# Optimization experiments

Hardware: AMD Instinct MI355X
Metric: run time of the kernel (lower is better)

Reference implementation:

```python
import jax, jax.numpy as jnp
import numpy as np

B_GRAPHS = 32   # number of graphs in the batch (static)
HEADS = 8
EPS = 1e-8


def _layer_norm(x, g, b):
    mu = x.mean(-1, keepdims=True)
    var = x.var(-1, keepdims=True)
    return (x - mu) * jax.lax.rsqrt(var + 1e-5) * g + b


def setup_inputs() -> dict:
    key = jax.random.key(0)
    ks = jax.random.split(key, 16)
    N, C, d, M = 5120, 128, 16, 256
    E = N * 16
    f32 = jnp.float32
    sc_c = 1.0 / np.sqrt(C)
    inp = {
        'x': jax.random.normal(ks[0], (N, C), f32),
        'pe_re': jax.random.normal(ks[1], (N, d), f32),
        'pe_im': jax.random.normal(ks[2], (N, d), f32),
        'wq': jax.random.normal(ks[3], (C, C), f32) * sc_c,
        'bq': jnp.zeros((C,), f32),
        'wk': jax.random.normal(ks[4], (C, C), f32) * sc_c,
        'bk': jnp.zeros((C,), f32),
        'wv': jax.random.normal(ks[5], (C, C), f32) * sc_c,
        'bv': jnp.zeros((C,), f32),
        'wo': jax.random.normal(ks[6], (C, C), f32) * sc_c,
        'bo': jnp.zeros((C,), f32),
        'pe_w1': jax.random.normal(ks[7], (4 * d, 2 * d), f32) * (1.0 / np.sqrt(4 * d)),
        'pe_b1': jnp.zeros((2 * d,), f32),
        'pe_w2': jax.random.normal(ks[8], (2 * d, HEADS), f32) * (1.0 / np.sqrt(2 * d)),
        'pe_b2': jnp.zeros((HEADS,), f32),
        'mlp_w1': jax.random.normal(ks[9], (C, 2 * C), f32) * sc_c,
        'mlp_b1': jnp.zeros((2 * C,), f32),
        'mlp_w2': jax.random.normal(ks[10], (2 * C, C), f32) * (1.0 / np.sqrt(2 * C)),
        'mlp_b2': jnp.zeros((C,), f32),
        'ln2_g': jnp.ones((C,), f32),
        'ln2_b': jnp.zeros((C,), f32),
        'ln3_g': jnp.ones((C,), f32),
        'ln3_b': jnp.zeros((C,), f32),
        'batch': jnp.sort(jax.random.randint(ks[11], (N,), 0, B_GRAPHS, jnp.int32)),
        'edge_index': jax.random.randint(ks[12], (2, E), 0, N, jnp.int32),
        'nmax': M,
    }
    return inp


def reference(x, pe_re, pe_im, wq, bq, wk, bk, wv, bv, wo, bo,
              pe_w1, pe_b1, pe_w2, pe_b2, mlp_w1, mlp_b1, mlp_w2, mlp_b2,
              ln2_g, ln2_b, ln3_g, ln3_b, batch, edge_index, nmax):
    N, C = x.shape
    H = HEADS
    dh = C // H
    M = nmax

    # --- to_dense_batch: ragged [N,*] -> dense [B, M, *] + mask ---
    counts = jax.ops.segment_sum(jnp.ones((N,), jnp.int32), batch, num_segments=B_GRAPHS)
    offsets = jnp.concatenate([jnp.zeros((1,), jnp.int32), jnp.cumsum(counts)[:-1]])
    intra = jnp.arange(N, dtype=jnp.int32) - offsets[batch]
    hd = jnp.zeros((B_GRAPHS, M, C), x.dtype).at[batch, intra].set(x)
    ar = jnp.zeros((B_GRAPHS, M, pe_re.shape[1]), x.dtype).at[batch, intra].set(pe_re)
    ai = jnp.zeros((B_GRAPHS, M, pe_im.shape[1]), x.dtype).at[batch, intra].set(pe_im)
    mask = jnp.zeros((B_GRAPHS, M), bool).at[batch, intra].set(True)

    # --- pairwise complex-angle PE bias ---
    pn = jnp.sqrt(ar * ar + ai * ai + EPS)                 # [B,M,d] complex_norm
    denom = pn[:, :, None, :] * pn[:, None, :, :] + EPS    # [B,M,M,d]
    # z_i * conj(z_j) normalized -> cos/sin of pairwise angle
    real = (ar[:, :, None, :] * ar[:, None, :, :] + ai[:, :, None, :] * ai[:, None, :, :]) / denom
    imag = (ai[:, :, None, :] * ar[:, None, :, :] - ar[:, :, None, :] * ai[:, None, :, :]) / denom
    pni = jnp.broadcast_to(pn[:, :, None, :], real.shape)
    pnj = jnp.broadcast_to(pn[:, None, :, :], real.shape)
    bias_in = jnp.concatenate([pni, pnj, real, imag], axis=-1)       # [B,M,M,4d]
    hb = jax.nn.relu(bias_in @ pe_w1 + pe_b1) @ pe_w2 + pe_b2        # [B,M,M,H]
    # torch: bias.transpose(1,-1) swaps dims 1 and 3 -> [B,H,M,M]
    bias = jnp.transpose(hb, (0, 3, 2, 1))                           # [B,H,q,k]

    # --- multi-head attention with float bias + key padding mask ---
    q = (hd @ wq + bq).reshape(B_GRAPHS, M, H, dh)
    k = (hd @ wk + bk).reshape(B_GRAPHS, M, H, dh)
    v = (hd @ wv + bv).reshape(B_GRAPHS, M, H, dh)
    scores = jnp.einsum('bihd,bjhd->bhij', q, k) / np.sqrt(dh) + bias
    scores = jnp.where(mask[:, None, None, :], scores, -1e9)
    attn = jax.nn.softmax(scores, axis=-1)
    o = jnp.einsum('bhij,bjhd->bihd', attn, v).reshape(B_GRAPHS, M, C)
    o = o @ wo + bo

    # --- back to ragged, residual, norms, FFN ---
    h = o[batch, intra] + x
    h = _layer_norm(h, ln2_g, ln2_b)
    out = h + (jax.nn.relu(h @ mlp_w1 + mlp_b1) @ mlp_w2 + mlp_b2)
    out = _layer_norm(out, ln3_g, ln3_b)
    return out
```

## Files before the change

kernel.cpp:

```cpp
#include <hip/hip_runtime.h>

#define N_NODES 5120
#define C_DIM   128
#define D_PE    16
#define M_MAX   256
#define B_G     32
#define H_HEADS 8
#define DH      16
#define EPS_PE  1e-8f
#define QT      4
#define SCP     264

#define WS_COUNTS   0
#define WS_OFFSETS  32
#define WS_INTRA    64
#define WS_MASK     5184
#define WS_HD       13376
#define WS_AR       1061952
#define WS_AI       1193024
#define WS_PN       1324096
#define WS_CN       1455168
#define WS_KFHI     1717312
#define WS_KFLO     1979456
#define WS_Q        2110528
#define WS_K        3159104
#define WS_V        4207680
#define WS_OATT     5256256
#define WS_OPROJ    6304832
#define WS_HLN      7353408
#define WS_FFNH     8008768
#define WS_FFNO     9319488
#define WS_BIAS     9974848
#define WS_ZERO_FLOATS 1324096

typedef __attribute__((ext_vector_type(8))) short bf8_t;
typedef __attribute__((ext_vector_type(4))) float f4_t;

__device__ inline short f2bf(float f) {
    union { float f; unsigned u; } v; v.f = f;
    unsigned r = (v.u + 0x7FFF + ((v.u >> 16) & 1)) >> 16;
    return (short)r;
}
__device__ inline float bf2f(short h) {
    union { unsigned u; float f; } v; v.u = ((unsigned)(unsigned short)h) << 16;
    return v.f;
}
__device__ inline unsigned pack2(short a, short b) {
    return (unsigned)(unsigned short)a | ((unsigned)(unsigned short)b << 16);
}
__device__ inline bf8_t bf8_from2(uint2 a, uint2 b) {
    bf8_t o;
    o[0]=(short)a.x; o[1]=(short)(a.x>>16); o[2]=(short)a.y; o[3]=(short)(a.y>>16);
    o[4]=(short)b.x; o[5]=(short)(b.x>>16); o[6]=(short)b.y; o[7]=(short)(b.y>>16);
    return o;
}

__global__ __launch_bounds__(256) void setup_kernel(
    const int* __restrict__ batch, int* __restrict__ offsets, int* __restrict__ intra)
{
    __shared__ int cnt[B_G];
    __shared__ int off[B_G];
    const int t = threadIdx.x;
    if (t < B_G) cnt[t] = 0;
    __syncthreads();
    for (int n = t; n < N_NODES; n += 256) atomicAdd(&cnt[batch[n]], 1);
    __syncthreads();
    if (t == 0) { int s = 0; for (int b = 0; b < B_G; ++b) { off[b] = s; s += cnt[b]; } }
    __syncthreads();
    if (t < B_G) offsets[t] = off[t];
    for (int n = t; n < N_NODES; n += 256) intra[n] = n - off[batch[n]];
}

__global__ __launch_bounds__(128) void scatter_kernel(
    const float* __restrict__ x, const float* __restrict__ pre, const float* __restrict__ pim,
    const int* __restrict__ batch, const int* __restrict__ intra,
    float* __restrict__ hd, float* __restrict__ ar, float* __restrict__ ai,
    int* __restrict__ mask)
{
    const int n = blockIdx.x, c = threadIdx.x;
    const int b = batch[n], m = intra[n];
    hd[((size_t)b * M_MAX + m) * C_DIM + c] = x[(size_t)n * C_DIM + c];
    if (c < D_PE) {
        ar[((size_t)b * M_MAX + m) * D_PE + c] = pre[(size_t)n * D_PE + c];
        ai[((size_t)b * M_MAX + m) * D_PE + c] = pim[(size_t)n * D_PE + c];
    }
    if (c == 0) mask[b * M_MAX + m] = 1;
}

__global__ __launch_bounds__(256) void prep_kernel(
    const float* __restrict__ ar, const float* __restrict__ ai,
    float* __restrict__ pn, float* __restrict__ cn,
    unsigned short* __restrict__ kf_hi, unsigned short* __restrict__ kf_lo)
{
    const int idx = blockIdx.x * 256 + threadIdx.x;
    const int cell = idx >> 4, dd = idx & 15;
    const float a = ar[idx], b = ai[idx];
    const float p = sqrtf(a * a + b * b + EPS_PE);
    const float inv = 1.f / p;
    const float cr = a * inv, ci = b * inv;
    pn[idx] = p;
    cn[(size_t)cell * 32 + dd]      = cr;
    cn[(size_t)cell * 32 + 16 + dd] = ci;
    const size_t hb = (size_t)cell * 64, lb = (size_t)cell * 32;
    short crh = f2bf(cr), cih = f2bf(ci);
    kf_hi[hb + dd]      = (unsigned short)crh;
    kf_hi[hb + 16 + dd] = (unsigned short)cih;
    kf_hi[hb + 32 + dd] = (unsigned short)f2bf(p);
    kf_hi[hb + 48 + dd] = (dd == 0) ? (unsigned short)f2bf(1.f) : 0;
    kf_lo[lb + dd]      = (unsigned short)f2bf(cr - bf2f(crh));
    kf_lo[lb + 16 + dd] = (unsigned short)f2bf(ci - bf2f(cih));
}

template<int K, int COUT, bool RELU, bool RES>
__global__ __launch_bounds__(256) void gemm_kernel(
    const float* __restrict__ A, const float* __restrict__ W,
    const float* __restrict__ bias, const float* __restrict__ res,
    float* __restrict__ out)
{
    __shared__ float sA[32 * K];
    const int r0 = blockIdx.x * 32;
    const int t = threadIdx.x;
    #pragma unroll
    for (int i = 0; i < (32 * K) / 256; ++i)
        sA[t + i * 256] = A[(size_t)r0 * K + t + i * 256];
    __syncthreads();

    constexpr int ROWS = (COUT == 128) ? 16 : 32;
    const int c  = (COUT == 128) ? (t & 127) : t;
    const int rg = (COUT == 128) ? (t >> 7) : 0;

    float acc[ROWS];
    #pragma unroll
    for (int r = 0; r < ROWS; ++r) acc[r] = 0.f;

    #pragma unroll 4
    for (int kk = 0; kk < K; ++kk) {
        float w = W[(size_t)kk * COUT + c];
        #pragma unroll
        for (int r = 0; r < ROWS; ++r)
            acc[r] = fmaf(sA[(rg * ROWS + r) * K + kk], w, acc[r]);
    }

    const float bv = bias[c];
    #pragma unroll
    for (int r = 0; r < ROWS; ++r) {
        const int row = r0 + rg * ROWS + r;
        float v = acc[r] + bv;
        if (RELU) v = fmaxf(v, 0.f);
        if (RES)  v += res[(size_t)row * COUT + c];
        out[(size_t)row * COUT + c] = v;
    }
}

__global__ __launch_bounds__(512) void bias_kernel(
    const float* __restrict__ cn, const float* __restrict__ pn,
    const unsigned short* __restrict__ kf_hi, const unsigned short* __restrict__ kf_lo,
    const float* __restrict__ w1, const float* __restrict__ b1,
    const float* __restrict__ w2, const float* __restrict__ b2,
    unsigned short* __restrict__ bias_out)
{
    __shared__ float sW1T[32][65];
    __shared__ float s_cn[16][32];
    __shared__ float s_pn[16][16];
    __shared__ uint2 s_scr[8][16][10];

    const int b  = blockIdx.y;
    const int i0 = blockIdx.x * 16;
    const int t  = threadIdx.x;

    for (int idx = t; idx < 2048; idx += 512) {
        int f = idx >> 5, hh = idx & 31;
        sW1T[hh][f] = w1[f * 32 + hh];
    }
    { int il = t >> 5, c = t & 31;
      s_cn[il][c] = cn[((size_t)(b * 256 + i0 + il)) * 32 + c]; }
    if (t < 256) { int il = t >> 4, dd = t & 15;
      s_pn[il][dd] = pn[((size_t)(b * 256 + i0 + il)) * 16 + dd]; }
    __syncthreads();

    const int w    = t >> 6;
    const int lane = t & 63;
    const int lj   = lane & 15;
    const int g    = lane >> 4;

    bf8_t a2f;
    #pragma unroll
    for (int e = 0; e < 8; ++e) {
        float v = (lj < 8) ? w2[(g * 8 + e) * 8 + lj] : 0.f;
        a2f[e] = f2bf(v);
    }
    float b2v0 = 0.f, b2v1 = 0.f, b2v2 = 0.f, b2v3 = 0.f;
    if (g < 2) { b2v0 = b2[g*4+0]; b2v1 = b2[g*4+1]; b2v2 = b2[g*4+2]; b2v3 = b2[g*4+3]; }

    for (int ii = 0; ii < 2; ++ii) {
        const int il = w * 2 + ii;
        const int i  = i0 + il;

        float vrow0 = b1[lj], vrow1 = b1[16 + lj];
        #pragma unroll
        for (int dd = 0; dd < 16; ++dd) {
            float p = s_pn[il][dd];
            vrow0 = fmaf(sW1T[lj][16 + dd],      p, vrow0);
            vrow1 = fmaf(sW1T[16 + lj][16 + dd], p, vrow1);
        }

        bf8_t a0hi0, a0lo0, a1f0, a0hi1, a0lo1, a1f1;
        #pragma unroll
        for (int e = 0; e < 8; ++e) {
            const int dd = (g & 1) * 8 + e;
            const float cr = s_cn[il][dd], ci = s_cn[il][16 + dd];
            {
                float wr = sW1T[lj][32 + dd], wi = sW1T[lj][48 + dd];
                float val = (g < 2) ? (wr * cr - wi * ci) : (wr * ci + wi * cr);
                short hi = f2bf(val);
                a0hi0[e] = hi; a0lo0[e] = f2bf(val - bf2f(hi));
                float v1 = (g < 2) ? sW1T[lj][g * 8 + e]
                                   : ((g == 2 && e == 0) ? vrow0 : 0.f);
                a1f0[e] = f2bf(v1);
            }
            {
                float wr = sW1T[16 + lj][32 + dd], wi = sW1T[16 + lj][48 + dd];
                float val = (g < 2) ? (wr * cr - wi * ci) : (wr * ci + wi * cr);
                short hi = f2bf(val);
                a0hi1[e] = hi; a0lo1[e] = f2bf(val - bf2f(hi));
                float v1 = (g < 2) ? sW1T[16 + lj][g * 8 + e]
                                   : ((g == 2 && e == 0) ? vrow1 : 0.f);
                a1f1[e] = f2bf(v1);
            }
        }

        for (int jt = 0; jt < 16; ++jt) {
            const size_t node = (size_t)b * 256 + jt * 16 + lj;
            const bf8_t* ph = (const bf8_t*)(kf_hi + node * 64);
            const bf8_t* pl = (const bf8_t*)(kf_lo + node * 32);
            bf8_t b0hi = ph[g];
            bf8_t b0lo = pl[g];
            bf8_t b1f  = ph[4 + g];

            f4_t acc0 = {0.f, 0.f, 0.f, 0.f}, acc1 = {0.f, 0.f, 0.f, 0.f};
            acc0 = __builtin_amdgcn_mfma_f32_16x16x32_bf16(a0hi0, b0hi, acc0, 0, 0, 0);
            acc0 = __builtin_amdgcn_mfma_f32_16x16x32_bf16(a0hi0, b0lo, acc0, 0, 0, 0);
            acc0 = __builtin_amdgcn_mfma_f32_16x16x32_bf16(a0lo0, b0hi, acc0, 0, 0, 0);
            acc0 = __builtin_amdgcn_mfma_f32_16x16x32_bf16(a1f0,  b1f,  acc0, 0, 0, 0);
            acc1 = __builtin_amdgcn_mfma_f32_16x16x32_bf16(a0hi1, b0hi, acc1, 0, 0, 0);
            acc1 = __builtin_amdgcn_mfma_f32_16x16x32_bf16(a0hi1, b0lo, acc1, 0, 0, 0);
            acc1 = __builtin_amdgcn_mfma_f32_16x16x32_bf16(a0lo1, b0hi, acc1, 0, 0, 0);
            acc1 = __builtin_amdgcn_mfma_f32_16x16x32_bf16(a1f1,  b1f,  acc1, 0, 0, 0);

            uint2 w0, w1p;
            w0.x  = pack2(f2bf(fmaxf(acc0[0], 0.f)), f2bf(fmaxf(acc0[1], 0.f)));
            w0.y  = pack2(f2bf(fmaxf(acc0[2], 0.f)), f2bf(fmaxf(acc0[3], 0.f)));
            w1p.x = pack2(f2bf(fmaxf(acc1[0], 0.f)), f2bf(fmaxf(acc1[1], 0.f)));
            w1p.y = pack2(f2bf(fmaxf(acc1[2], 0.f)), f2bf(fmaxf(acc1[3], 0.f)));
            s_scr[w][lj][g]     = w0;
            s_scr[w][lj][4 + g] = w1p;
            __builtin_amdgcn_s_waitcnt(0);

            uint2 q0 = s_scr[w][lj][2 * g];
            uint2 q1 = s_scr[w][lj][2 * g + 1];
            bf8_t hb = bf8_from2(q0, q1);

            f4_t acc2 = {0.f, 0.f, 0.f, 0.f};
            acc2 = __builtin_amdgcn_mfma_f32_16x16x32_bf16(a2f, hb, acc2, 0, 0, 0);

            if (g < 2) {
                uint2 st;
                st.x = pack2(f2bf(acc2[0] + b2v0), f2bf(acc2[1] + b2v1));
                st.y = pack2(f2bf(acc2[2] + b2v2), f2bf(acc2[3] + b2v3));
                size_t idx = (((size_t)b * 256 + i) * 256 + jt * 16 + lj) * 8 + g * 4;
                *(uint2*)(bias_out + idx) = st;
            }
        }
    }
}

__global__ __launch_bounds__(256) void attn_kernel(
    const float* __restrict__ qm, const float* __restrict__ km, const float* __restrict__ vm,
    const int* __restrict__ mask, const unsigned short* __restrict__ bias,
    float* __restrict__ o_att)
{
    const int b  = blockIdx.y;
    const int i0 = blockIdx.x * QT;
    const int t  = threadIdx.x;
    const int j  = t;

    __shared__ float s_q[QT][C_DIM];
    __shared__ float s_sc[QT][H_HEADS][SCP];

    for (int idx = t; idx < QT * C_DIM; idx += 256) {
        const int qi = idx >> 7, c = idx & 127;
        s_q[qi][c] = qm[((size_t)(b * 256 + i0 + qi)) * C_DIM + c];
    }
    __syncthreads();

    const int mj = mask[b * M_MAX + j];
    uint4 bu[QT];
    #pragma unroll
    for (int qi = 0; qi < QT; ++qi)
        bu[qi] = *(const uint4*)(bias + (((size_t)(b * 256 + i0 + qi)) * 256 + j) * 8);

    const float* krow = km + ((size_t)(b * 256 + j)) * C_DIM;
    #pragma unroll
    for (int h = 0; h < 8; ++h) {
        float kv[DH];
        #pragma unroll
        for (int q4 = 0; q4 < 4; ++q4) {
            float4 v = ((const float4*)(krow + h * DH))[q4];
            kv[q4*4+0]=v.x; kv[q4*4+1]=v.y; kv[q4*4+2]=v.z; kv[q4*4+3]=v.w;
        }
        #pragma unroll
        for (int qi = 0; qi < QT; ++qi) {
            float dot = 0.f;
            #pragma unroll
            for (int dd = 0; dd < DH; ++dd)
                dot = fmaf(s_q[qi][h * DH + dd], kv[dd], dot);
            const unsigned u = ((const unsigned*)&bu[qi])[h >> 1];
            const float bv = bf2f((short)((h & 1) ? (u >> 16) : (u & 0xffff)));
            s_sc[qi][h][j] = mj ? fmaf(dot, 0.25f, bv) : -1e9f;
        }
    }
    __syncthreads();

    {
        const int wave = t >> 6, lane = t & 63;
        for (int r = wave; r < QT * H_HEADS; r += 4) {
            float* row = ((float*)s_sc) + r * SCP;
            float x0 = row[lane], x1 = row[lane + 64], x2 = row[lane + 128], x3 = row[lane + 192];
            float mx = fmaxf(fmaxf(x0, x1), fmaxf(x2, x3));
            #pragma unroll
            for (int off = 32; off > 0; off >>= 1) mx = fmaxf(mx, __shfl_xor(mx, off, 64));
            float e0 = expf(x0 - mx), e1 = expf(x1 - mx), e2 = expf(x2 - mx), e3 = expf(x3 - mx);
            float s = e0 + e1 + e2 + e3;
            #pragma unroll
            for (int off = 32; off > 0; off >>= 1) s += __shfl_xor(s, off, 64);
            const float inv = 1.f / s;
            row[lane] = e0 * inv; row[lane + 64] = e1 * inv;
            row[lane + 128] = e2 * inv; row[lane + 192] = e3 * inv;
        }
    }
    __syncthreads();

    {
        const int c = t & 127;
        const int gq = t >> 7;
        const int h = c >> 4;
        const int qA = gq * 2, qB = gq * 2 + 1;
        const float* vb = vm + (size_t)b * M_MAX * C_DIM + c;
        float a0 = 0.f, a1 = 0.f;
        for (int jj = 0; jj < M_MAX; jj += 4) {
            float4 pA = *(const float4*)&s_sc[qA][h][jj];
            float4 pB = *(const float4*)&s_sc[qB][h][jj];
            float v0 = vb[(size_t)(jj + 0) * C_DIM];
            float v1 = vb[(size_t)(jj + 1) * C_DIM];
            float v2 = vb[(size_t)(jj + 2) * C_DIM];
            float v3 = vb[(size_t)(jj + 3) * C_DIM];
            a0 = fmaf(pA.x, v0, a0); a0 = fmaf(pA.y, v1, a0);
            a0 = fmaf(pA.z, v2, a0); a0 = fmaf(pA.w, v3, a0);
            a1 = fmaf(pB.x, v0, a1); a1 = fmaf(pB.y, v1, a1);
            a1 = fmaf(pB.z, v2, a1); a1 = fmaf(pB.w, v3, a1);
        }
        o_att[((size_t)(b * 256 + i0 + qA)) * C_DIM + c] = a0;
        o_att[((size_t)(b * 256 + i0 + qB)) * C_DIM + c] = a1;
    }
}

__global__ __launch_bounds__(128) void gather_res_ln_kernel(
    const float* __restrict__ op, const float* __restrict__ x,
    const int* __restrict__ batch, const int* __restrict__ intra,
    const float* __restrict__ g, const float* __restrict__ be, float* __restrict__ out)
{
    const int n = blockIdx.x, c = threadIdx.x;
    const int b = batch[n], m = intra[n];
    const float v = op[((size_t)b * M_MAX + m) * C_DIM + c] + x[(size_t)n * C_DIM + c];
    float s = v, sq = v * v;
    #pragma unroll
    for (int off = 32; off > 0; off >>= 1) {
        s  += __shfl_xor(s, off, 64);
        sq += __shfl_xor(sq, off, 64);
    }
    __shared__ float red[4];
    if ((threadIdx.x & 63) == 0) {
        red[(threadIdx.x >> 6) * 2]     = s;
        red[(threadIdx.x >> 6) * 2 + 1] = sq;
    }
    __syncthreads();
    s = red[0] + red[2]; sq = red[1] + red[3];
    const float mu  = s * (1.f / C_DIM);
    const float var = sq * (1.f / C_DIM) - mu * mu;
    const float sc  = rsqrtf(var + 1e-5f);
    out[(size_t)n * C_DIM + c] = (v - mu) * sc * g[c] + be[c];
}

__global__ __launch_bounds__(128) void ln_kernel(
    const float* __restrict__ in, const float* __restrict__ g,
    const float* __restrict__ be, float* __restrict__ out)
{
    const int n = blockIdx.x, c = threadIdx.x;
    const float v = in[(size_t)n * C_DIM + c];
    float s = v, sq = v * v;
    #pragma unroll
    for (int off = 32; off > 0; off >>= 1) {
        s  += __shfl_xor(s, off, 64);
        sq += __shfl_xor(sq, off, 64);
    }
    __shared__ float red[4];
    if ((threadIdx.x & 63) == 0) {
        red[(threadIdx.x >> 6) * 2]     = s;
        red[(threadIdx.x >> 6) * 2 + 1] = sq;
    }
    __syncthreads();
    s = red[0] + red[2]; sq = red[1] + red[3];
    const float mu  = s * (1.f / C_DIM);
    const float var = sq * (1.f / C_DIM) - mu * mu;
    const float sc  = rsqrtf(var + 1e-5f);
    out[(size_t)n * C_DIM + c] = (v - mu) * sc * g[c] + be[c];
}

extern "C" void kernel_launch(void* const* d_in, const int* in_sizes, int n_in,
                              void* d_out, int out_size, void* d_ws, size_t ws_size,
                              hipStream_t stream)
{
    const float* x      = (const float*)d_in[0];
    const float* pe_re  = (const float*)d_in[1];
    const float* pe_im  = (const float*)d_in[2];
    const float* wq     = (const float*)d_in[3];
    const float* bq     = (const float*)d_in[4];
    const float* wk     = (const float*)d_in[5];
    const float* bk     = (const float*)d_in[6];
    const float* wv     = (const float*)d_in[7];
    const float* bv     = (const float*)d_in[8];
    const float* wo     = (const float*)d_in[9];
    const float* bo     = (const float*)d_in[10];
    const float* pe_w1  = (const float*)d_in[11];
    const float* pe_b1  = (const float*)d_in[12];
    const float* pe_w2  = (const float*)d_in[13];
    const float* pe_b2  = (const float*)d_in[14];
    const float* mlp_w1 = (const float*)d_in[15];
    const float* mlp_b1 = (const float*)d_in[16];
    const float* mlp_w2 = (const float*)d_in[17];
    const float* mlp_b2 = (const float*)d_in[18];
    const float* ln2_g  = (const float*)d_in[19];
    const float* ln2_b  = (const float*)d_in[20];
    const float* ln3_g  = (const float*)d_in[21];
    const float* ln3_b  = (const float*)d_in[22];
    const int*   batch  = (const int*)d_in[23];

    float* ws = (float*)d_ws;
    int*   offsets = (int*)(ws + WS_OFFSETS);
    int*   intra   = (int*)(ws + WS_INTRA);
    int*   mask    = (int*)(ws + WS_MASK);
    float* hd   = ws + WS_HD;
    float* ar   = ws + WS_AR;
    float* ai   = ws + WS_AI;
    float* pn   = ws + WS_PN;
    float* cn   = ws + WS_CN;
    unsigned short* kf_hi = (unsigned short*)(ws + WS_KFHI);
    unsigned short* kf_lo = (unsigned short*)(ws + WS_KFLO);
    float* qm   = ws + WS_Q;
    float* km   = ws + WS_K;
    float* vm   = ws + WS_V;
    float* oatt = ws + WS_OATT;
    float* oprj = ws + WS_OPROJ;
    float* hln  = ws + WS_HLN;
    float* ffnh = ws + WS_FFNH;
    float* ffno = ws + WS_FFNO;
    unsigned short* bias = (unsigned short*)(ws + WS_BIAS);
    float* outp = (float*)d_out;

    hipMemsetAsync(d_ws, 0, (size_t)WS_ZERO_FLOATS * sizeof(float), stream);

    setup_kernel<<<1, 256, 0, stream>>>(batch, offsets, intra);
    scatter_kernel<<<N_NODES, 128, 0, stream>>>(x, pe_re, pe_im, batch, intra, hd, ar, ai, mask);
    prep_kernel<<<512, 256, 0, stream>>>(ar, ai, pn, cn, kf_hi, kf_lo);

    gemm_kernel<128, 128, false, false><<<256, 256, 0, stream>>>(hd, wq, bq, nullptr, qm);
    gemm_kernel<128, 128, false, false><<<256, 256, 0, stream>>>(hd, wk, bk, nullptr, km);
    gemm_kernel<128, 128, false, false><<<256, 256, 0, stream>>>(hd, wv, bv, nullptr, vm);

    bias_kernel<<<dim3(16, 32), 512, 0, stream>>>(cn, pn, kf_hi, kf_lo,
                                                  pe_w1, pe_b1, pe_w2, pe_b2, bias);

    attn_kernel<<<dim3(M_MAX / QT, B_G), 256, 0, stream>>>(qm, km, vm, mask, bias, oatt);

    gemm_kernel<128, 128, false, false><<<256, 256, 0, stream>>>(oatt, wo, bo, nullptr, oprj);
    gather_res_ln_kernel<<<N_NODES, 128, 0, stream>>>(oprj, x, batch, intra, ln2_g, ln2_b, hln);
    gemm_kernel<128, 256, true,  false><<<160, 256, 0, stream>>>(hln, mlp_w1, mlp_b1, nullptr, ffnh);
    gemm_kernel<256, 128, false, true ><<<160, 256, 0, stream>>>(ffnh, mlp_w2, mlp_b2, hln, ffno);
    ln_kernel<<<N_NODES, 128, 0, stream>>>(ffno, ln3_g, ln3_b, outp);
}
```

Before: 335.5 us.

## Replace scalar FP32 GEMMs with split-bf16 MFMA GEMMs and fuse QKV launch

```diff
diff --git a/kernel.cpp b/kernel.cpp
--- a/kernel.cpp
+++ b/kernel.cpp
@@ -31,7 +31,16 @@
 #define WS_FFNH     8008768
 #define WS_FFNO     9319488
 #define WS_BIAS     9974848
+#define WS_WPK_HI   18363456
+#define WS_WPK_LO   18428992
 #define WS_ZERO_FLOATS 1324096
+
+#define WOFF_Q   0
+#define WOFF_K   16384
+#define WOFF_V   32768
+#define WOFF_O   49152
+#define WOFF_W1  65536
+#define WOFF_W2  98304
 
 typedef __attribute__((ext_vector_type(8))) short bf8_t;
 typedef __attribute__((ext_vector_type(4))) float f4_t;
@@ -111,45 +120,112 @@
     kf_lo[lb + 16 + dd] = (unsigned short)f2bf(ci - bf2f(cih));
 }
 
-template<int K, int COUT, bool RELU, bool RES>
-__global__ __launch_bounds__(256) void gemm_kernel(
-    const float* __restrict__ A, const float* __restrict__ W,
+__global__ __launch_bounds__(256) void wpack_kernel(
+    const float* __restrict__ wq, const float* __restrict__ wk,
+    const float* __restrict__ wv, const float* __restrict__ wo,
+    const float* __restrict__ w1, const float* __restrict__ w2,
+    unsigned short* __restrict__ hi, unsigned short* __restrict__ lo)
+{
+    const int tid = blockIdx.x * 256 + threadIdx.x;
+    const int tile = tid >> 6, lane = tid & 63;
+    const float* W; int N, ltile; size_t off;
+    if (tile < 128) {
+        const int wi = tile >> 5; ltile = tile & 31; N = 128;
+        W = (wi == 0) ? wq : (wi == 1) ? wk : (wi == 2) ? wv : wo;
+        off = (size_t)wi * 16384;
+    } else if (tile < 192) { ltile = tile - 128; N = 256; W = w1; off = WOFF_W1; }
+    else                   { ltile = tile - 192; N = 128; W = w2; off = WOFF_W2; }
+    const int NT = N / 16;
+    const int kt = ltile / NT, nt = ltile % NT;
+    const int col = nt * 16 + (lane & 15);
+    const int k0  = kt * 32 + (lane >> 4) * 8;
+    bf8_t vhi, vlo;
+    #pragma unroll
+    for (int e = 0; e < 8; ++e) {
+        const float v = W[(size_t)(k0 + e) * N + col];
+        const short h = f2bf(v);
+        vhi[e] = h; vlo[e] = f2bf(v - bf2f(h));
+    }
+    const size_t toff = off + ((size_t)ltile * 64 + lane) * 8;
+    *(bf8_t*)(hi + toff) = vhi;
+    *(bf8_t*)(lo + toff) = vlo;
+}
+
+template<int K, int N, bool RELU, bool RES>
+__device__ inline void mgemm_body(
+    const float* __restrict__ A, const unsigned short* __restrict__ hi,
+    const unsigned short* __restrict__ lo,
     const float* __restrict__ bias, const float* __restrict__ res,
-    float* __restrict__ out)
-{
-    __shared__ float sA[32 * K];
-    const int r0 = blockIdx.x * 32;
-    const int t = threadIdx.x;
-    #pragma unroll
-    for (int i = 0; i < (32 * K) / 256; ++i)
-        sA[t + i * 256] = A[(size_t)r0 * K + t + i * 256];
-    __syncthreads();
-
-    constexpr int ROWS = (COUT == 128) ? 16 : 32;
-    const int c  = (COUT == 128) ? (t & 127) : t;
-    const int rg = (COUT == 128) ? (t >> 7) : 0;
-
-    float acc[ROWS];
-    #pragma unroll
-    for (int r = 0; r < ROWS; ++r) acc[r] = 0.f;
-
-    #pragma unroll 4
-    for (int kk = 0; kk < K; ++kk) {
-        float w = W[(size_t)kk * COUT + c];
-        #pragma unroll
-        for (int r = 0; r < ROWS; ++r)
-            acc[r] = fmaf(sA[(rg * ROWS + r) * K + kk], w, acc[r]);
-    }
-
-    const float bv = bias[c];
-    #pragma unroll
-    for (int r = 0; r < ROWS; ++r) {
-        const int row = r0 + rg * ROWS + r;
-        float v = acc[r] + bv;
-        if (RELU) v = fmaxf(v, 0.f);
-        if (RES)  v += res[(size_t)row * COUT + c];
-        out[(size_t)row * COUT + c] = v;
-    }
+    float* __restrict__ out, int bx)
+{
+    constexpr int NT = N / 16, KT = K / 32;
+    const int rb = bx * 64;
+    const int w = threadIdx.x >> 6, lane = threadIdx.x & 63;
+    const int arow = rb + w * 16 + (lane & 15);
+    const int g = lane >> 4;
+
+    f4_t acc[NT];
+    #pragma unroll
+    for (int nt = 0; nt < NT; ++nt) acc[nt] = (f4_t){0.f, 0.f, 0.f, 0.f};
+
+    #pragma unroll
+    for (int kt = 0; kt < KT; ++kt) {
+        const float* ap = A + (size_t)arow * K + kt * 32 + g * 8;
+        const float4 a0 = *(const float4*)ap;
+        const float4 a1 = *(const float4*)(ap + 4);
+        const float av[8] = {a0.x, a0.y, a0.z, a0.w, a1.x, a1.y, a1.z, a1.w};
+        bf8_t ahi, alo;
+        #pragma unroll
+        for (int e = 0; e < 8; ++e) {
+            const short h = f2bf(av[e]);
+            ahi[e] = h; alo[e] = f2bf(av[e] - bf2f(h));
+        }
+        #pragma unroll
+        for (int nt = 0; nt < NT; ++nt) {
+            const size_t toff = ((size_t)(kt * NT + nt) * 64 + lane) * 8;
+            const bf8_t bhi = *(const bf8_t*)(hi + toff);
+            const bf8_t blo = *(const bf8_t*)(lo + toff);
+            acc[nt] = __builtin_amdgcn_mfma_f32_16x16x32_bf16(ahi, bhi, acc[nt], 0, 0, 0);
+            acc[nt] = __builtin_amdgcn_mfma_f32_16x16x32_bf16(alo, bhi, acc[nt], 0, 0, 0);
+            acc[nt] = __builtin_amdgcn_mfma_f32_16x16x32_bf16(ahi, blo, acc[nt], 0, 0, 0);
+        }
+    }
+
+    const int orow0 = rb + w * 16 + g * 4;
+    #pragma unroll
+    for (int nt = 0; nt < NT; ++nt) {
+        const int col = nt * 16 + (lane & 15);
+        const float bv = bias[col];
+        #pragma unroll
+        for (int r = 0; r < 4; ++r) {
+            float v = acc[nt][r] + bv;
+            if (RELU) v = fmaxf(v, 0.f);
+            if (RES)  v += res[(size_t)(orow0 + r) * N + col];
+            out[(size_t)(orow0 + r) * N + col] = v;
+        }
+    }
+}
+
+__global__ __launch_bounds__(256) void qkv_kernel(
+    const float* __restrict__ A,
+    const unsigned short* __restrict__ hi, const unsigned short* __restrict__ lo,
+    const float* __restrict__ bq, const float* __restrict__ bk, const float* __restrict__ bv,
+    float* __restrict__ qm, float* __restrict__ km, float* __restrict__ vm)
+{
+    const int sel = blockIdx.y;
+    const float* bias = (sel == 0) ? bq : (sel == 1) ? bk : bv;
+    float* out = (sel == 0) ? qm : (sel == 1) ? km : vm;
+    const size_t woff = (size_t)sel * 16384;
+    mgemm_body<128, 128, false, false>(A, hi + woff, lo + woff, bias, nullptr, out, blockIdx.x);
+}
+
+template<int K, int N, bool RELU, bool RES>
+__global__ __launch_bounds__(256) void mgemm_kernel(
+    const float* __restrict__ A,
+    const unsigned short* __restrict__ hi, const unsigned short* __restrict__ lo,
+    const float* __restrict__ bias, const float* __restrict__ res, float* __restrict__ out)
+{
+    mgemm_body<K, N, RELU, RES>(A, hi, lo, bias, res, out, blockIdx.x);
 }
 
 __global__ __launch_bounds__(512) void bias_kernel(
@@ -465,26 +541,30 @@
     float* ffnh = ws + WS_FFNH;
     float* ffno = ws + WS_FFNO;
     unsigned short* bias = (unsigned short*)(ws + WS_BIAS);
+    unsigned short* wpk_hi = (unsigned short*)(ws + WS_WPK_HI);
+    unsigned short* wpk_lo = (unsigned short*)(ws + WS_WPK_LO);
     float* outp = (float*)d_out;
 
     hipMemsetAsync(d_ws, 0, (size_t)WS_ZERO_FLOATS * sizeof(float), stream);
 
     setup_kernel<<<1, 256, 0, stream>>>(batch, offsets, intra);
+    wpack_kernel<<<64, 256, 0, stream>>>(wq, wk, wv, wo, mlp_w1, mlp_w2, wpk_hi, wpk_lo);
     scatter_kernel<<<N_NODES, 128, 0, stream>>>(x, pe_re, pe_im, batch, intra, hd, ar, ai, mask);
     prep_kernel<<<512, 256, 0, stream>>>(ar, ai, pn, cn, kf_hi, kf_lo);
 
-    gemm_kernel<128, 128, false, false><<<256, 256, 0, stream>>>(hd, wq, bq, nullptr, qm);
-    gemm_kernel<128, 128, false, false><<<256, 256, 0, stream>>>(hd, wk, bk, nullptr, km);
-    gemm_kernel<128, 128, false, false><<<256, 256, 0, stream>>>(hd, wv, bv, nullptr, vm);
+    qkv_kernel<<<dim3(128, 3), 256, 0, stream>>>(hd, wpk_hi, wpk_lo, bq, bk, bv, qm, km, vm);
 
     bias_kernel<<<dim3(16, 32), 512, 0, stream>>>(cn, pn, kf_hi, kf_lo,
                                                   pe_w1, pe_b1, pe_w2, pe_b2, bias);
 
     attn_kernel<<<dim3(M_MAX / QT, B_G), 256, 0, stream>>>(qm, km, vm, mask, bias, oatt);
 
-    gemm_kernel<128, 128, false, false><<<256, 256, 0, stream>>>(oatt, wo, bo, nullptr, oprj);
+    mgemm_kernel<128, 128, false, false><<<128, 256, 0, stream>>>(
+        oatt, wpk_hi + WOFF_O, wpk_lo + WOFF_O, bo, nullptr, oprj);
     gather_res_ln_kernel<<<N_NODES, 128, 0, stream>>>(oprj, x, batch, intra, ln2_g, ln2_b, hln);
-    gemm_kernel<128, 256, true,  false><<<160, 256, 0, stream>>>(hln, mlp_w1, mlp_b1, nullptr, ffnh);
-    gemm_kernel<256, 128, false, true ><<<160, 256, 0, stream>>>(ffnh, mlp_w2, mlp_b2, hln, ffno);
+    mgemm_kernel<128, 256, true, false><<<80, 256, 0, stream>>>(
+        hln, wpk_hi + WOFF_W1, wpk_lo + WOFF_W1, mlp_b1, nullptr, ffnh);
+    mgemm_kernel<256, 128, false, true><<<80, 256, 0, stream>>>(
+        ffnh, wpk_hi + WOFF_W2, wpk_lo + WOFF_W2, mlp_b2, hln, ffno);
     ln_kernel<<<N_NODES, 128, 0, stream>>>(ffno, ln3_g, ln3_b, outp);
 }
```

After: 315.1 us. 1.06x faster.
